# Optimization experiments

Hardware: AMD Instinct MI355X
Metric: run time of the kernel (lower is better)

## Reference

```python
import jax, jax.numpy as jnp
import numpy as np

N_NODES = 8192
IN_FEATS, H_FEATS, NUM_CLASSES = 512, 256, 16


def _glorot(key, shape):
    fan_in, fan_out = shape[0], shape[1]
    limit = float(np.sqrt(6.0 / (fan_in + fan_out)))
    return jax.random.uniform(key, shape, jnp.float32, -limit, limit)


def setup_inputs() -> dict:
    key = jax.random.key(0)
    ks = jax.random.split(key, 16)
    return {
        "x": jax.random.normal(ks[0], (N_NODES, IN_FEATS), jnp.float32),
        "w1": _glorot(ks[1], (IN_FEATS, H_FEATS)), "b1": jnp.zeros((H_FEATS,), jnp.float32),
        "w2": _glorot(ks[2], (H_FEATS, H_FEATS)), "b2": jnp.zeros((H_FEATS,), jnp.float32),
        "w3": _glorot(ks[3], (H_FEATS, 32)),      "b3": jnp.zeros((32,), jnp.float32),
        "t": _glorot(ks[4], (1, 1)), "theta": _glorot(ks[5], (1, 1)),
        "gw1": _glorot(ks[6], (32, 16)), "gb1": jnp.zeros((16,), jnp.float32),
        "gw2": _glorot(ks[7], (16, 8)),  "gb2": jnp.zeros((8,), jnp.float32),
        "lw1": _glorot(ks[8], (8, 16)),  "lb1": jnp.zeros((16,), jnp.float32),
        "lw2": _glorot(ks[9], (16, NUM_CLASSES)), "lb2": jnp.zeros((NUM_CLASSES,), jnp.float32),
    }


def _pairwise_dist(h):
    # Euclidean cdist(h, h): [N, N], stable sqrt with zero subgradient at d=0
    sq = jnp.sum(h * h, axis=1)
    d2 = jnp.maximum(sq[:, None] + sq[None, :] - 2.0 * (h @ h.T), 0.0)
    return jnp.where(d2 > 0.0, jnp.sqrt(jnp.where(d2 > 0.0, d2, 1.0)), 0.0)


def reference(x, w1, b1, w2, b2, w3, b3, t, theta, gw1, gb1, gw2, gb2, lw1, lb1, lw2, lb2):
    n = x.shape[0]
    # MLP encoder (dropout is eval-mode identity)
    h = jax.nn.relu(x @ w1 + b1)
    h = jax.nn.relu(h @ w2 + b2)
    h = h @ w3 + b3                                  # [N, 32]
    # latent dense graph: A = sigmoid(t * (cdist + theta)); all entries > 0 -> fully dense graph
    A = jax.nn.sigmoid(t[0, 0] * (_pairwise_dist(h) + theta[0, 0]))   # [N, N]
    inv_deg = 1.0 / n                                # norm='right', in-degree == N for dense graph
    # GraphConv: dst aggregates sum_src A[src,dst] * (h[src] @ W) then right-normalizes
    h = jax.nn.relu((A.T @ (h @ gw1)) * inv_deg + gb1)   # [N, 16]
    h = jax.nn.relu((A.T @ (h @ gw2)) * inv_deg + gb2)   # [N, 8]
    h = jax.nn.relu(h @ lw1 + lb1)
    return h @ lw2 + lb2                             # [N, num_classes]
```

## Files before the change

kernel.cpp:

```cpp
#include <hip/hip_runtime.h>

typedef __attribute__((ext_vector_type(8))) short short8;
typedef __attribute__((ext_vector_type(4))) float f32x4;
typedef __attribute__((ext_vector_type(2))) unsigned int u32x2;
typedef unsigned short u16;
typedef unsigned int u32;

#define MFMA16 __builtin_amdgcn_mfma_f32_16x16x32_bf16

__device__ __forceinline__ u16 f2bf(float f) {
    u32 u = __builtin_bit_cast(u32, f);
    return (u16)((u + 0x7FFFu + ((u >> 16) & 1u)) >> 16);
}

__device__ __forceinline__ void split2(float f, u16& hi, u16& lo) {
    u32 u = __builtin_bit_cast(u32, f);
    hi = (u16)(u >> 16);
    float hf = __builtin_bit_cast(float, u & 0xFFFF0000u);
    float r = f - hf;
    lo = (u16)(__builtin_bit_cast(u32, r) >> 16);
}

__device__ __forceinline__ int swzA(int row, int slot) {
    return row * 64 + ((slot ^ ((row >> 1) & 3)) << 4);
}

__global__ void __launch_bounds__(256) k_tr(const float* __restrict__ w, float* __restrict__ wt,
                                            int K, int N) {
    int idx = blockIdx.x * 256 + threadIdx.x;
    if (idx >= K * N) return;
    int k = idx / N, n = idx - k * N;
    wt[n * K + k] = w[idx];
}

template <int K, int BN, bool RELU>
__global__ void __launch_bounds__(256, 2) k_gemm(const float* __restrict__ A,
                                                 const float* __restrict__ Bt,
                                                 const float* __restrict__ bias,
                                                 float* __restrict__ C, const int N) {
    constexpr int NT = BN / 16;
    __shared__ __align__(16) char smem[16384];
    char* const Ah = smem;
    char* const Al = smem + 4096;
    char* const Bh = smem + 8192;
    char* const Bl = smem + 12288;
    const int tid = threadIdx.x, lane = tid & 63, w = tid >> 6;
    const int frow = lane & 15, fg = lane >> 4;
    const int m0 = blockIdx.x * 64, n0 = blockIdx.y * BN;
    const int srow = tid >> 2, sc = tid & 3;
    const int swa = swzA(srow, sc);
    const bool doB = (BN == 64) || (tid < 128);
    const float* gA = A + (m0 + srow) * K + sc * 8;
    const float* gB = Bt + (n0 + srow) * K + sc * 8;

    f32x4 acc[NT];
    float bv[NT];
#pragma unroll
    for (int nt = 0; nt < NT; nt++) {
        acc[nt] = {0.f, 0.f, 0.f, 0.f};
        bv[nt] = bias[n0 + nt * 16 + frow];
    }
    const int fra = swzA(w * 16 + frow, fg);
    int frb[NT];
#pragma unroll
    for (int nt = 0; nt < NT; nt++) frb[nt] = swzA(nt * 16 + frow, fg);

    for (int k0 = 0; k0 < K; k0 += 32) {
        f32x4 a0 = *(const f32x4*)(gA + k0);
        f32x4 a1 = *(const f32x4*)(gA + k0 + 4);
        f32x4 b0 = {0.f, 0.f, 0.f, 0.f}, b1 = {0.f, 0.f, 0.f, 0.f};
        if (doB) {
            b0 = *(const f32x4*)(gB + k0);
            b1 = *(const f32x4*)(gB + k0 + 4);
        }
        __syncthreads();
        {
            short8 ah8, al8;
#pragma unroll
            for (int i = 0; i < 4; i++) { u16 hh, ll; split2(a0[i], hh, ll); ah8[i] = (short)hh; al8[i] = (short)ll; }
#pragma unroll
            for (int i = 0; i < 4; i++) { u16 hh, ll; split2(a1[i], hh, ll); ah8[4 + i] = (short)hh; al8[4 + i] = (short)ll; }
            *(short8*)(Ah + swa) = ah8;
            *(short8*)(Al + swa) = al8;
        }
        if (doB) {
            short8 bh8, bl8;
#pragma unroll
            for (int i = 0; i < 4; i++) { u16 hh, ll; split2(b0[i], hh, ll); bh8[i] = (short)hh; bl8[i] = (short)ll; }
#pragma unroll
            for (int i = 0; i < 4; i++) { u16 hh, ll; split2(b1[i], hh, ll); bh8[4 + i] = (short)hh; bl8[4 + i] = (short)ll; }
            *(short8*)(Bh + swa) = bh8;
            *(short8*)(Bl + swa) = bl8;
        }
        __syncthreads();
        const short8 afh = *(const short8*)(Ah + fra);
        const short8 afl = *(const short8*)(Al + fra);
#pragma unroll
        for (int nt = 0; nt < NT; nt++) {
            const short8 bfh = *(const short8*)(Bh + frb[nt]);
            const short8 bfl = *(const short8*)(Bl + frb[nt]);
            acc[nt] = MFMA16(afh, bfh, acc[nt], 0, 0, 0);
            acc[nt] = MFMA16(afh, bfl, acc[nt], 0, 0, 0);
            acc[nt] = MFMA16(afl, bfh, acc[nt], 0, 0, 0);
        }
    }
#pragma unroll
    for (int nt = 0; nt < NT; nt++) {
#pragma unroll
        for (int r = 0; r < 4; r++) {
            float v = acc[nt][r] + bv[nt];
            if (RELU) v = fmaxf(v, 0.f);
            C[(m0 + w * 16 + fg * 4 + r) * N + (n0 + nt * 16 + frow)] = v;
        }
    }
}

__global__ void __launch_bounds__(256) k_post(const float* __restrict__ H,
                                              const float* __restrict__ gw1,
                                              u16* __restrict__ hhi, u16* __restrict__ hlo,
                                              float* __restrict__ sqv, u16* __restrict__ B1t) {
    __shared__ float gs[512];
    const int tid = threadIdx.x;
    gs[tid] = gw1[tid];
    gs[tid + 256] = gw1[tid + 256];
    __syncthreads();
    const int j = blockIdx.x * 256 + tid;
    float h[32];
#pragma unroll
    for (int q = 0; q < 8; q++) {
        f32x4 v = *(const f32x4*)(H + j * 32 + q * 4);
        h[q * 4 + 0] = v[0]; h[q * 4 + 1] = v[1]; h[q * 4 + 2] = v[2]; h[q * 4 + 3] = v[3];
    }
    float s = 0.f;
#pragma unroll
    for (int k = 0; k < 32; k++) s = fmaf(h[k], h[k], s);
    sqv[j] = s;
#pragma unroll
    for (int q = 0; q < 4; q++) {
        short8 vh, vl;
#pragma unroll
        for (int e = 0; e < 8; e++) {
            u16 hh, ll;
            split2(h[q * 8 + e], hh, ll);
            vh[e] = (short)hh; vl[e] = (short)ll;
        }
        *(short8*)(hhi + j * 32 + q * 8) = vh;
        *(short8*)(hlo + j * 32 + q * 8) = vl;
    }
    const float inv = 0.0001220703125f;
#pragma unroll
    for (int f = 0; f < 16; f++) {
        float a = 0.f;
#pragma unroll
        for (int k = 0; k < 32; k++) a = fmaf(h[k], gs[k * 16 + f], a);
        B1t[f * 8192 + j] = f2bf(a * inv);
    }
}

__device__ __forceinline__ void ew_pack(char* astr, int awoff, const f32x4 s, const f32x4 sq4,
                                        float sq_i, float c0, float c1, int jloc, int il_cmp) {
    float p[4];
#pragma unroll
    for (int r = 0; r < 4; r++) {
        float d2 = fmaf(s[r], -2.f, sq_i + sq4[r]);
        d2 = fmaxf(d2, 0.f);
        float d = __builtin_amdgcn_sqrtf(d2);
        if (jloc + r == il_cmp) d = 0.f;
        const float z = fmaf(d, c1, c0);
        p[r] = __builtin_amdgcn_rcpf(1.f + __builtin_amdgcn_exp2f(z));
    }
    u32 w0, w1;
    asm("v_cvt_pk_bf16_f32 %0, %1, %2" : "=v"(w0) : "v"(p[0]), "v"(p[1]));
    asm("v_cvt_pk_bf16_f32 %0, %1, %2" : "=v"(w1) : "v"(p[2]), "v"(p[3]));
    u32x2 pk = {w0, w1};
    *(u32x2*)(astr + awoff) = pk;
}

__global__ void __launch_bounds__(256) k_agg(const u16* __restrict__ hhi, const u16* __restrict__ hlo,
                                             const float* __restrict__ sqv, const u16* __restrict__ Bt,
                                             float* __restrict__ P,
                                             const float* __restrict__ tp, const float* __restrict__ thp) {
    __shared__ __align__(16) char smem[16640];
    char* const bufh = smem;
    char* const bufl = smem + 4096;
    float* const sqb = (float*)(smem + 8192);
    char* const astr0 = smem + 8448;

    const int tid = threadIdx.x, lane = tid & 63, w = tid >> 6;
    const int frow = lane & 15, fg = lane >> 4;
    const int dstbase = blockIdx.x * 64;
    const int chunk = blockIdx.y;
    const float t = tp[0], th = thp[0];
    const float c1 = -t * 1.44269504088896340736f;
    const float c0 = c1 * th;
    char* const astr = astr0 + w * 2048;

    const int srow = tid >> 2, sc = tid & 3;
    const int swa = swzA(srow, sc);

    const int igf = dstbase + w * 16 + frow;
    const short8 hdh = *(const short8*)(hhi + igf * 32 + fg * 8);
    const short8 hdl = *(const short8*)(hlo + igf * 32 + fg * 8);
    const float sq_i = sqv[igf];
    const int il = w * 16 + frow;

    int awo[4], ard[2];
#pragma unroll
    for (int jj = 0; jj < 4; jj++)
        awo[jj] = frow * 128 + (((2 * jj + (fg >> 1)) ^ (frow & 7)) << 4) + ((fg & 1) << 3);
#pragma unroll
    for (int h = 0; h < 2; h++) ard[h] = frow * 128 + (((4 * h + fg) ^ (frow & 7)) << 4);

    f32x4 outacc = {0.f, 0.f, 0.f, 0.f};

    const int jb0 = chunk * 16 * 64;
    short8 pvh = *(const short8*)(hhi + (jb0 + srow) * 32 + sc * 8);
    short8 pvl = *(const short8*)(hlo + (jb0 + srow) * 32 + sc * 8);
    float psq = 0.f;
    if (tid < 64) psq = sqv[jb0 + tid];

    for (int jtl = 0; jtl < 16; ++jtl) {
        const int jbase = (chunk * 16 + jtl) * 64;
        __syncthreads();
        *(short8*)(bufh + swa) = pvh;
        *(short8*)(bufl + swa) = pvl;
        if (tid < 64) sqb[tid] = psq;
        if (jtl + 1 < 16) {
            const int jn = jbase + 64;
            pvh = *(const short8*)(hhi + (jn + srow) * 32 + sc * 8);
            pvl = *(const short8*)(hlo + (jn + srow) * 32 + sc * 8);
            if (tid < 64) psq = sqv[jn + tid];
        }
        __syncthreads();
        const int il_cmp = (jbase == dstbase) ? il : -1;
#pragma unroll
        for (int h = 0; h < 2; ++h) {
            const short8 hs0h = *(const short8*)(bufh + swzA(h * 32 + frow, fg));
            const short8 hs0l = *(const short8*)(bufl + swzA(h * 32 + frow, fg));
            const short8 hs1h = *(const short8*)(bufh + swzA(h * 32 + 16 + frow, fg));
            const short8 hs1l = *(const short8*)(bufl + swzA(h * 32 + 16 + frow, fg));
            const f32x4 sq0 = *(const f32x4*)(sqb + h * 32 + fg * 4);
            const f32x4 sq1 = *(const f32x4*)(sqb + h * 32 + 16 + fg * 4);
            const short8 bfh = *(const short8*)(Bt + frow * 8192 + jbase + h * 32 + fg * 8);
            f32x4 s0 = {0.f, 0.f, 0.f, 0.f}, s1 = {0.f, 0.f, 0.f, 0.f};
            s0 = MFMA16(hs0h, hdh, s0, 0, 0, 0);
            s0 = MFMA16(hs0h, hdl, s0, 0, 0, 0);
            s0 = MFMA16(hs0l, hdh, s0, 0, 0, 0);
            s1 = MFMA16(hs1h, hdh, s1, 0, 0, 0);
            s1 = MFMA16(hs1h, hdl, s1, 0, 0, 0);
            s1 = MFMA16(hs1l, hdh, s1, 0, 0, 0);
            ew_pack(astr, awo[2 * h], s0, sq0, sq_i, c0, c1, (2 * h) * 16 + fg * 4, il_cmp);
            ew_pack(astr, awo[2 * h + 1], s1, sq1, sq_i, c0, c1, (2 * h + 1) * 16 + fg * 4, il_cmp);
            const short8 af = *(const short8*)(astr + ard[h]);
            outacc = MFMA16(af, bfh, outacc, 0, 0, 0);
        }
    }
#pragma unroll
    for (int r = 0; r < 4; r++) {
        const int ig = dstbase + w * 16 + fg * 4 + r;
        P[(chunk * 8192 + ig) * 16 + frow] = outacc[r];
    }
}

__global__ void __launch_bounds__(256) k_reduce1(const float* __restrict__ P,
                                                 const float* __restrict__ gw2,
                                                 const float* __restrict__ gb1,
                                                 u16* __restrict__ B2t) {
    __shared__ float gs[128];
    const int tid = threadIdx.x;
    if (tid < 128) gs[tid] = gw2[tid];
    __syncthreads();
    const int j = blockIdx.x * 256 + tid;
    float g[16];
#pragma unroll
    for (int q = 0; q < 4; q++) {
        f32x4 v = *(const f32x4*)(P + j * 16 + q * 4);
        g[q * 4 + 0] = v[0]; g[q * 4 + 1] = v[1]; g[q * 4 + 2] = v[2]; g[q * 4 + 3] = v[3];
    }
#pragma unroll
    for (int c = 1; c < 8; c++) {
#pragma unroll
        for (int q = 0; q < 4; q++) {
            f32x4 v = *(const f32x4*)(P + (c * 8192 + j) * 16 + q * 4);
            g[q * 4 + 0] += v[0]; g[q * 4 + 1] += v[1]; g[q * 4 + 2] += v[2]; g[q * 4 + 3] += v[3];
        }
    }
#pragma unroll
    for (int f = 0; f < 16; f++) g[f] = fmaxf(g[f] + gb1[f], 0.f);
    const float inv = 0.0001220703125f;
#pragma unroll
    for (int f2 = 0; f2 < 8; f2++) {
        float a = 0.f;
#pragma unroll
        for (int k = 0; k < 16; k++) a = fmaf(g[k], gs[k * 8 + f2], a);
        B2t[f2 * 8192 + j] = f2bf(a * inv);
    }
#pragma unroll
    for (int f2 = 8; f2 < 16; f2++) B2t[f2 * 8192 + j] = 0;
}

__global__ void __launch_bounds__(256) k_final(const float* __restrict__ P,
                                               const float* __restrict__ gb2,
                                               const float* __restrict__ lw1,
                                               const float* __restrict__ lb1,
                                               const float* __restrict__ lw2,
                                               const float* __restrict__ lb2,
                                               float* __restrict__ out) {
    __shared__ float s1[128], s2[256];
    const int tid = threadIdx.x;
    if (tid < 128) s1[tid] = lw1[tid];
    s2[tid] = lw2[tid];
    __syncthreads();
    const int j = blockIdx.x * 256 + tid;
    float g[8];
#pragma unroll
    for (int q = 0; q < 2; q++) {
        f32x4 v = *(const f32x4*)(P + j * 16 + q * 4);
        g[q * 4 + 0] = v[0]; g[q * 4 + 1] = v[1]; g[q * 4 + 2] = v[2]; g[q * 4 + 3] = v[3];
    }
#pragma unroll
    for (int c = 1; c < 8; c++) {
#pragma unroll
        for (int q = 0; q < 2; q++) {
            f32x4 v = *(const f32x4*)(P + (c * 8192 + j) * 16 + q * 4);
            g[q * 4 + 0] += v[0]; g[q * 4 + 1] += v[1]; g[q * 4 + 2] += v[2]; g[q * 4 + 3] += v[3];
        }
    }
#pragma unroll
    for (int f = 0; f < 8; f++) g[f] = fmaxf(g[f] + gb2[f], 0.f);
    float l1[16];
#pragma unroll
    for (int f = 0; f < 16; f++) {
        float a = lb1[f];
#pragma unroll
        for (int k = 0; k < 8; k++) a = fmaf(g[k], s1[k * 16 + f], a);
        l1[f] = fmaxf(a, 0.f);
    }
#pragma unroll
    for (int q = 0; q < 4; q++) {
        f32x4 v;
#pragma unroll
        for (int e = 0; e < 4; e++) {
            const int f = q * 4 + e;
            float a = lb2[f];
#pragma unroll
            for (int k = 0; k < 16; k++) a = fmaf(l1[k], s2[k * 16 + f], a);
            v[e] = a;
        }
        *(f32x4*)(out + j * 16 + q * 4) = v;
    }
}

extern "C" void kernel_launch(void* const* d_in, const int* in_sizes, int n_in,
                              void* d_out, int out_size, void* d_ws, size_t ws_size,
                              hipStream_t stream) {
    (void)in_sizes; (void)n_in; (void)out_size; (void)ws_size;
    const float* x   = (const float*)d_in[0];
    const float* w1  = (const float*)d_in[1];
    const float* b1  = (const float*)d_in[2];
    const float* w2  = (const float*)d_in[3];
    const float* b2  = (const float*)d_in[4];
    const float* w3  = (const float*)d_in[5];
    const float* b3  = (const float*)d_in[6];
    const float* t   = (const float*)d_in[7];
    const float* th  = (const float*)d_in[8];
    const float* gw1 = (const float*)d_in[9];
    const float* gb1 = (const float*)d_in[10];
    const float* gw2 = (const float*)d_in[11];
    const float* gb2 = (const float*)d_in[12];
    const float* lw1 = (const float*)d_in[13];
    const float* lb1 = (const float*)d_in[14];
    const float* lw2 = (const float*)d_in[15];
    const float* lb2 = (const float*)d_in[16];

    char* ws = (char*)d_ws;
    float* wt1 = (float*)(ws + 0);
    float* wt2 = (float*)(ws + 524288);
    float* wt3 = (float*)(ws + 786432);
    float* H1  = (float*)(ws + 819200);
    float* P   = (float*)(ws + 819200);
    float* H2  = (float*)(ws + 9207808);
    float* H   = (float*)(ws + 17596416);
    u16*   hhi = (u16*)(ws + 18644992);
    u16*   hlo = (u16*)(ws + 19169280);
    float* sqv = (float*)(ws + 19693568);
    u16*   B1t = (u16*)(ws + 19726336);
    u16*   B2t = (u16*)(ws + 19988480);

    k_tr<<<(512 * 256 + 255) / 256, 256, 0, stream>>>(w1, wt1, 512, 256);
    k_tr<<<(256 * 256 + 255) / 256, 256, 0, stream>>>(w2, wt2, 256, 256);
    k_tr<<<(256 * 32 + 255) / 256, 256, 0, stream>>>(w3, wt3, 256, 32);

    k_gemm<512, 64, true ><<<dim3(128, 4), 256, 0, stream>>>(x,  wt1, b1, H1, 256);
    k_gemm<256, 64, true ><<<dim3(128, 4), 256, 0, stream>>>(H1, wt2, b2, H2, 256);
    k_gemm<256, 32, false><<<dim3(128, 1), 256, 0, stream>>>(H2, wt3, b3, H, 32);

    k_post<<<32, 256, 0, stream>>>(H, gw1, hhi, hlo, sqv, B1t);

    k_agg<<<dim3(128, 8), 256, 0, stream>>>(hhi, hlo, sqv, B1t, P, t, th);
    k_reduce1<<<32, 256, 0, stream>>>(P, gw2, gb1, B2t);
    k_agg<<<dim3(128, 8), 256, 0, stream>>>(hhi, hlo, sqv, B2t, P, t, th);
    k_final<<<32, 256, 0, stream>>>(P, gb2, lw1, lb1, lw2, lb2, (float*)d_out);
}
```

Baseline: 135.6 us.

## Double-buffer LDS tiles in k_agg, double chunk split, specialize diagonal tiles

The aggregation kernel now double-buffers the source h tiles and squared norms in LDS. This lets the next tile be stored while the current one is consumed, with a single barrier per iteration instead of two. The source dimension is split into 16 chunks instead of 8, doubling the grid to expose more parallelism. The reduce kernels are updated to sum 16 partials, which doubles partial-buffer traffic. The diagonal-zeroing compare is templated so that non-diagonal tiles skip it.

```diff
diff --git a/kernel.cpp b/kernel.cpp
--- a/kernel.cpp
+++ b/kernel.cpp
@@ -7,6 +7,9 @@
 typedef unsigned int u32;
 
 #define MFMA16 __builtin_amdgcn_mfma_f32_16x16x32_bf16
+
+constexpr int NCH = 16;
+constexpr int NJT = 8192 / 64 / NCH;
 
 __device__ __forceinline__ u16 f2bf(float f) {
     u32 u = __builtin_bit_cast(u32, f);
@@ -157,15 +160,18 @@
     }
 }
 
+template <bool DIAG>
 __device__ __forceinline__ void ew_pack(char* astr, int awoff, const f32x4 s, const f32x4 sq4,
-                                        float sq_i, float c0, float c1, int jloc, int il_cmp) {
+                                        float sq_i, float c0, float c1, int jloc, int il) {
     float p[4];
 #pragma unroll
     for (int r = 0; r < 4; r++) {
         float d2 = fmaf(s[r], -2.f, sq_i + sq4[r]);
         d2 = fmaxf(d2, 0.f);
         float d = __builtin_amdgcn_sqrtf(d2);
-        if (jloc + r == il_cmp) d = 0.f;
+        if (DIAG) {
+            if (jloc + r == il) d = 0.f;
+        }
         const float z = fmaf(d, c1, c0);
         p[r] = __builtin_amdgcn_rcpf(1.f + __builtin_amdgcn_exp2f(z));
     }
@@ -180,11 +186,11 @@
                                              const float* __restrict__ sqv, const u16* __restrict__ Bt,
                                              float* __restrict__ P,
                                              const float* __restrict__ tp, const float* __restrict__ thp) {
-    __shared__ __align__(16) char smem[16640];
+    __shared__ __align__(16) char smem[25088];
     char* const bufh = smem;
-    char* const bufl = smem + 4096;
-    float* const sqb = (float*)(smem + 8192);
-    char* const astr0 = smem + 8448;
+    char* const bufl = smem + 8192;
+    float* const sqb = (float*)(smem + 16384);
+    char* const astr0 = smem + 16896;
 
     const int tid = threadIdx.x, lane = tid & 63, w = tid >> 6;
     const int frow = lane & 15, fg = lane >> 4;
@@ -213,34 +219,47 @@
 
     f32x4 outacc = {0.f, 0.f, 0.f, 0.f};
 
-    const int jb0 = chunk * 16 * 64;
-    short8 pvh = *(const short8*)(hhi + (jb0 + srow) * 32 + sc * 8);
-    short8 pvl = *(const short8*)(hlo + (jb0 + srow) * 32 + sc * 8);
-    float psq = 0.f;
-    if (tid < 64) psq = sqv[jb0 + tid];
-
-    for (int jtl = 0; jtl < 16; ++jtl) {
-        const int jbase = (chunk * 16 + jtl) * 64;
+    const int jt0 = chunk * NJT;
+    short8 pvh = *(const short8*)(hhi + ((jt0 * 64) + srow) * 32 + sc * 8);
+    short8 pvl = *(const short8*)(hlo + ((jt0 * 64) + srow) * 32 + sc * 8);
+    float psq = (tid < 64) ? sqv[jt0 * 64 + tid] : 0.f;
+    *(short8*)(bufh + swa) = pvh;
+    *(short8*)(bufl + swa) = pvl;
+    if (tid < 64) sqb[tid] = psq;
+    if (NJT > 1) {
+        const int jn = (jt0 + 1) * 64;
+        pvh = *(const short8*)(hhi + (jn + srow) * 32 + sc * 8);
+        pvl = *(const short8*)(hlo + (jn + srow) * 32 + sc * 8);
+        if (tid < 64) psq = sqv[jn + tid];
+    }
+
+    for (int it = 0; it < NJT; ++it) {
+        const int b = it & 1;
+        const int jbase = (jt0 + it) * 64;
         __syncthreads();
-        *(short8*)(bufh + swa) = pvh;
-        *(short8*)(bufl + swa) = pvl;
-        if (tid < 64) sqb[tid] = psq;
-        if (jtl + 1 < 16) {
-            const int jn = jbase + 64;
+        if (it + 1 < NJT) {
+            *(short8*)(bufh + (b ^ 1) * 4096 + swa) = pvh;
+            *(short8*)(bufl + (b ^ 1) * 4096 + swa) = pvl;
+            if (tid < 64) sqb[(b ^ 1) * 64 + tid] = psq;
+        }
+        if (it + 2 < NJT) {
+            const int jn = (jt0 + it + 2) * 64;
             pvh = *(const short8*)(hhi + (jn + srow) * 32 + sc * 8);
             pvl = *(const short8*)(hlo + (jn + srow) * 32 + sc * 8);
             if (tid < 64) psq = sqv[jn + tid];
         }
-        __syncthreads();
-        const int il_cmp = (jbase == dstbase) ? il : -1;
+        char* const bh = bufh + b * 4096;
+        char* const bl = bufl + b * 4096;
+        const float* sqp = sqb + b * 64;
+        const bool diag = (jbase == dstbase);
 #pragma unroll
         for (int h = 0; h < 2; ++h) {
-            const short8 hs0h = *(const short8*)(bufh + swzA(h * 32 + frow, fg));
-            const short8 hs0l = *(const short8*)(bufl + swzA(h * 32 + frow, fg));
-            const short8 hs1h = *(const short8*)(bufh + swzA(h * 32 + 16 + frow, fg));
-            const short8 hs1l = *(const short8*)(bufl + swzA(h * 32 + 16 + frow, fg));
-            const f32x4 sq0 = *(const f32x4*)(sqb + h * 32 + fg * 4);
-            const f32x4 sq1 = *(const f32x4*)(sqb + h * 32 + 16 + fg * 4);
+            const short8 hs0h = *(const short8*)(bh + swzA(h * 32 + frow, fg));
+            const short8 hs0l = *(const short8*)(bl + swzA(h * 32 + frow, fg));
+            const short8 hs1h = *(const short8*)(bh + swzA(h * 32 + 16 + frow, fg));
+            const short8 hs1l = *(const short8*)(bl + swzA(h * 32 + 16 + frow, fg));
+            const f32x4 sq0 = *(const f32x4*)(sqp + h * 32 + fg * 4);
+            const f32x4 sq1 = *(const f32x4*)(sqp + h * 32 + 16 + fg * 4);
             const short8 bfh = *(const short8*)(Bt + frow * 8192 + jbase + h * 32 + fg * 8);
             f32x4 s0 = {0.f, 0.f, 0.f, 0.f}, s1 = {0.f, 0.f, 0.f, 0.f};
             s0 = MFMA16(hs0h, hdh, s0, 0, 0, 0);
@@ -249,8 +268,13 @@
             s1 = MFMA16(hs1h, hdh, s1, 0, 0, 0);
             s1 = MFMA16(hs1h, hdl, s1, 0, 0, 0);
             s1 = MFMA16(hs1l, hdh, s1, 0, 0, 0);
-            ew_pack(astr, awo[2 * h], s0, sq0, sq_i, c0, c1, (2 * h) * 16 + fg * 4, il_cmp);
-            ew_pack(astr, awo[2 * h + 1], s1, sq1, sq_i, c0, c1, (2 * h + 1) * 16 + fg * 4, il_cmp);
+            if (diag) {
+                ew_pack<true>(astr, awo[2 * h], s0, sq0, sq_i, c0, c1, (2 * h) * 16 + fg * 4, il);
+                ew_pack<true>(astr, awo[2 * h + 1], s1, sq1, sq_i, c0, c1, (2 * h + 1) * 16 + fg * 4, il);
+            } else {
+                ew_pack<false>(astr, awo[2 * h], s0, sq0, sq_i, c0, c1, 0, -1);
+                ew_pack<false>(astr, awo[2 * h + 1], s1, sq1, sq_i, c0, c1, 0, -1);
+            }
             const short8 af = *(const short8*)(astr + ard[h]);
             outacc = MFMA16(af, bfh, outacc, 0, 0, 0);
         }
@@ -278,7 +302,7 @@
         g[q * 4 + 0] = v[0]; g[q * 4 + 1] = v[1]; g[q * 4 + 2] = v[2]; g[q * 4 + 3] = v[3];
     }
 #pragma unroll
-    for (int c = 1; c < 8; c++) {
+    for (int c = 1; c < NCH; c++) {
 #pragma unroll
         for (int q = 0; q < 4; q++) {
             f32x4 v = *(const f32x4*)(P + (c * 8192 + j) * 16 + q * 4);
@@ -319,7 +343,7 @@
         g[q * 4 + 0] = v[0]; g[q * 4 + 1] = v[1]; g[q * 4 + 2] = v[2]; g[q * 4 + 3] = v[3];
     }
 #pragma unroll
-    for (int c = 1; c < 8; c++) {
+    for (int c = 1; c < NCH; c++) {
 #pragma unroll
         for (int q = 0; q < 2; q++) {
             f32x4 v = *(const f32x4*)(P + (c * 8192 + j) * 16 + q * 4);
@@ -397,8 +421,8 @@
 
     k_post<<<32, 256, 0, stream>>>(H, gw1, hhi, hlo, sqv, B1t);
 
-    k_agg<<<dim3(128, 8), 256, 0, stream>>>(hhi, hlo, sqv, B1t, P, t, th);
+    k_agg<<<dim3(128, NCH), 256, 0, stream>>>(hhi, hlo, sqv, B1t, P, t, th);
     k_reduce1<<<32, 256, 0, stream>>>(P, gw2, gb1, B2t);
-    k_agg<<<dim3(128, 8), 256, 0, stream>>>(hhi, hlo, sqv, B2t, P, t, th);
+    k_agg<<<dim3(128, NCH), 256, 0, stream>>>(hhi, hlo, sqv, B2t, P, t, th);
     k_final<<<32, 256, 0, stream>>>(P, gb2, lw1, lb1, lw2, lb2, (float*)d_out);
 }
```

Result: faster. 131.5 us (-3.0%).
